# Optimization experiments

Hardware: AMD Instinct MI355X
Metric: run time of the kernel (lower is better)

## Reference

```python
import jax, jax.numpy as jnp
import numpy as np

ALPHA = 0.2  # LeakyReLU negative slope


def setup_inputs() -> dict:
    key = jax.random.key(0)
    k1, k2, k3, k4 = jax.random.split(key, 4)
    B, N, F_IN, F_OUT = 4, 4096, 256, 256
    h = jax.random.normal(k1, (B, N, F_IN), dtype=jnp.float32)
    adj = jax.random.randint(k2, (B, N, N), 0, 2, dtype=jnp.int32)
    # xavier_normal with gain=1.414: std = gain*sqrt(2/(fan_in+fan_out))
    std_W = 1.414 * np.sqrt(2.0 / (F_IN + F_OUT))
    W = jax.random.normal(k3, (F_IN, F_OUT), dtype=jnp.float32) * std_W
    std_a = 1.414 * np.sqrt(2.0 / (1 + 2 * F_OUT))
    a = jax.random.normal(k4, (1, 2 * F_OUT), dtype=jnp.float32) * std_a
    return {"h": h, "adj": adj, "W": W, "a": a}


def reference(h, adj, W, a):
    # h: [B, N, F_in], adj: [B, N, N] (0/1), W: [F_in, F_out], a: [1, 2*F_out]
    F_out = W.shape[1]
    Hh = jnp.einsum('bni,io->bno', h, W)               # [B, N, F_out]
    a_src = a[0, :F_out]                                # attends to edge source i
    a_dst = a[0, F_out:]                                # attends to edge target j
    s = jnp.einsum('bno,o->bn', Hh, a_src)              # [B, N]
    d = jnp.einsum('bno,o->bn', Hh, a_dst)              # [B, N]
    # score(i,j) = a . concat(Hh_i, Hh_j) = s_i + d_j
    logits = s[:, :, None] + d[:, None, :]              # [B, N, N]
    # edge_e = exp(-leakyrelu(score)) only on edges (adj nonzero), else 0
    e = jnp.where(adj != 0,
                  jnp.exp(-jax.nn.leaky_relu(logits, negative_slope=ALPHA)),
                  jnp.zeros((), dtype=Hh.dtype))        # [B, N, N]
    rowsum = jnp.sum(e, axis=-1, keepdims=True)         # [B, N, 1]
    # rows with zero sum keep divisor 1 (as in the torch code)
    rowsum = jnp.where(rowsum == 0.0, 1.0, rowsum)
    h_prime = jnp.einsum('bnm,bmo->bno', e, Hh) / rowsum  # [B, N, F_out]
    return jax.nn.elu(h_prime)  # concat=True branch
```

## Files before the change

### kernel.cpp

```cpp
#include <hip/hip_runtime.h>

#define LRELU_ALPHA 0.2f

typedef __bf16 bf16x8 __attribute__((ext_vector_type(8)));
typedef unsigned short u16;
typedef unsigned short u16x4v __attribute__((ext_vector_type(4)));
typedef unsigned short u16x8 __attribute__((ext_vector_type(8)));
typedef float f32x4 __attribute__((ext_vector_type(4)));
typedef int int4v __attribute__((ext_vector_type(4)));
typedef unsigned int u32;

__device__ __forceinline__ u16 f2bf(float f) {
  unsigned int u = __float_as_uint(f);
  u += 0x7fffu + ((u >> 16) & 1u);
  return (u16)(u >> 16);
}

__device__ __forceinline__ void gload16(const void* g, void* lds) {
  __builtin_amdgcn_global_load_lds(
      (const __attribute__((address_space(1))) void*)g,
      (__attribute__((address_space(3))) void*)lds, 16, 0, 0);
}

__global__ __launch_bounds__(256) void wcast(const float* __restrict__ W,
                                             u16* __restrict__ WbT) {
  int idx = blockIdx.x * 256 + threadIdx.x;
  WbT[idx] = f2bf(W[(idx & 255) * 256 + (idx >> 8)]);
}

__global__ __launch_bounds__(256) void packadj(const int* __restrict__ adj,
                                               u32* __restrict__ maskg) {
  __shared__ unsigned char nib[1024];
  const int tid = threadIdx.x;
  const size_t row0 = (size_t)blockIdx.x * 8;
  for (int rr = 0; rr < 8; ++rr) {
    const size_t row = row0 + rr;
    const int* arow = adj + row * 4096;
    for (int it = 0; it < 4; ++it) {
      int4v v = *(const int4v*)(arow + it * 1024 + tid * 4);
      unsigned char nb = (unsigned char)((v.x != 0) | ((v.y != 0) << 1) |
                                         ((v.z != 0) << 2) | ((v.w != 0) << 3));
      nib[tid] = nb;
      __syncthreads();
      if (tid < 32) {
        const u32* nw = (const u32*)nib;
        u32 w0 = nw[tid * 2], w1 = nw[tid * 2 + 1];
        u32 m = (w0 & 0xFu) | ((w0 >> 4) & 0xF0u) | ((w0 >> 8) & 0xF00u) |
                ((w0 >> 12) & 0xF000u);
        m |= ((w1 & 0xFu) | ((w1 >> 4) & 0xF0u) | ((w1 >> 8) & 0xF00u) |
              ((w1 >> 12) & 0xF000u)) << 16;
        maskg[row * 128 + it * 32 + tid] = m;
      }
      __syncthreads();
    }
  }
}

__global__ __launch_bounds__(256) void gemm1(const float* __restrict__ h,
                                             const u16* __restrict__ WbT,
                                             const float* __restrict__ a,
                                             u16* __restrict__ HhTt,
                                             float* __restrict__ sbuf,
                                             float* __restrict__ dbuf) {
  const int tid = threadIdx.x, bid = blockIdx.x;
  const int l = tid & 63, w = tid >> 6;
  const int lr = l & 15;
  const int lk = (l >> 4) << 3;
  const int rowA = bid * 64 + 16 * w + lr;
  const float* hrow = h + (size_t)rowA * 256 + lk;

  f32x4 acc[16];
#pragma unroll
  for (int n = 0; n < 16; ++n) acc[n] = (f32x4){0.f, 0.f, 0.f, 0.f};

  for (int k0 = 0; k0 < 256; k0 += 32) {
    f32x4 a0 = *(const f32x4*)(hrow + k0);
    f32x4 a1 = *(const f32x4*)(hrow + k0 + 4);
    u16x8 au;
    au[0] = f2bf(a0[0]); au[1] = f2bf(a0[1]); au[2] = f2bf(a0[2]); au[3] = f2bf(a0[3]);
    au[4] = f2bf(a1[0]); au[5] = f2bf(a1[1]); au[6] = f2bf(a1[2]); au[7] = f2bf(a1[3]);
    bf16x8 af = __builtin_bit_cast(bf16x8, au);
#pragma unroll
    for (int n = 0; n < 16; ++n) {
      int4v bv = *(const int4v*)(WbT + (size_t)(16 * n + lr) * 256 + k0 + lk);
      bf16x8 bf = __builtin_bit_cast(bf16x8, bv);
      acc[n] = __builtin_amdgcn_mfma_f32_16x16x32_bf16(af, bf, acc[n], 0, 0, 0);
    }
  }

  float sp[4] = {0.f, 0.f, 0.f, 0.f}, dp[4] = {0.f, 0.f, 0.f, 0.f};
#pragma unroll
  for (int n = 0; n < 16; ++n) {
    int col = 16 * n + lr;
    float as = a[col];
    float ad = a[256 + col];
#pragma unroll
    for (int rr = 0; rr < 4; ++rr) {
      int row = bid * 64 + 16 * w + ((l >> 4) << 2) + rr;
      int bb = row >> 12, kk = row & 4095;
      float v = acc[n][rr];
      size_t addr = (size_t)bb * 1048576 + (size_t)(kk >> 5) * 8192 +
                    (col >> 4) * 512 + ((kk >> 3) & 3) * 128 + (col & 15) * 8 +
                    (kk & 7);
      HhTt[addr] = f2bf(v);
      sp[rr] += v * as;
      dp[rr] += v * ad;
    }
  }
#pragma unroll
  for (int rr = 0; rr < 4; ++rr) {
#pragma unroll
    for (int off = 1; off < 16; off <<= 1) {
      sp[rr] += __shfl_xor(sp[rr], off);
      dp[rr] += __shfl_xor(dp[rr], off);
    }
  }
  if ((l & 15) == 0) {
#pragma unroll
    for (int rr = 0; rr < 4; ++rr) {
      int row = bid * 64 + 16 * w + ((l >> 4) << 2) + rr;
      sbuf[row] = sp[rr];
      dbuf[row] = dp[rr];
    }
  }
}

__global__ __launch_bounds__(512, 2) void gat_main(const u32* __restrict__ maskg,
                                                   const u16* __restrict__ HhTt,
                                                   const float* __restrict__ s,
                                                   const float* __restrict__ d,
                                                   float* __restrict__ out) {
  __shared__ __align__(16) u16 Bt[4][8192];
  __shared__ __align__(16) u16 At[2][2048];
  __shared__ __align__(16) u32 Mk[8192];
  __shared__ __align__(16) float Dl[4096];
  __shared__ float rs_lds[64];

  const int tid = threadIdx.x, bid = blockIdx.x;
  const int xcd = bid & 7;
  const int t256 = (xcd << 5) | (bid >> 3);
  const int b = t256 >> 6;
  const int rowbase = (t256 & 63) << 6;

  const int l = tid & 63, w = tid >> 6;
  const int lr = l & 15, lkg = l >> 4;
  const int wr = w & 1, wc = w >> 1;

  for (int i = tid; i < 1024; i += 512)
    *(f32x4*)&Dl[i * 4] = *(const f32x4*)(d + b * 4096 + i * 4);
  {
    const u32* mrow = maskg + (size_t)(b * 4096 + rowbase) * 128;
    int r = tid >> 3, w0 = (tid & 7) * 16;
#pragma unroll
    for (int j = 0; j < 16; ++j) {
      int ww = w0 + j;
      Mk[r * 128 + ((ww + r) & 127)] = mrow[r * 128 + ww];
    }
  }

  const int er = tid >> 3, c8 = tid & 7;
  const float s_e = s[b * 4096 + rowbase + er];

  const char* bsrc0 = (const char*)HhTt +
      ((size_t)b * 1048576 + (2 * w + 0) * 512 + l * 8) * 2;
  const char* bsrc1 = (const char*)HhTt +
      ((size_t)b * 1048576 + (2 * w + 1) * 512 + l * 8) * 2;
  char* BtB = (char*)&Bt[0][0];

  const int atoff0 = (32 * wr + lr) * 32 + lkg * 8;
  const int atoff1 = (32 * wr + 16 + lr) * 32 + lkg * 8;
  const int btoff = 4 * wc * 512 + lkg * 128 + lr * 8;

  f32x4 acc0[4], acc1[4];
#pragma unroll
  for (int n = 0; n < 4; ++n) {
    acc0[n] = (f32x4){0.f, 0.f, 0.f, 0.f};
    acc1[n] = (f32x4){0.f, 0.f, 0.f, 0.f};
  }
  float racc = 0.f;

#define ISSUE(BUF, STEP)                                                      \
  {                                                                           \
    const size_t so_ = (size_t)(STEP) * 16384;                                \
    gload16(bsrc0 + so_, BtB + (BUF) * 16384 + (2 * w + 0) * 1024);           \
    gload16(bsrc1 + so_, BtB + (BUF) * 16384 + (2 * w + 1) * 1024);           \
  }

#define EGEN(BUFA, STEP)                                                      \
  {                                                                           \
    const int st_ = (STEP);                                                   \
    u32 mword = Mk[er * 128 + ((st_ + er) & 127)];                            \
    u32 m8 = mword >> (c8 * 4);                                               \
    f32x4 dv = *(const f32x4*)&Dl[st_ * 32 + c8 * 4];                         \
    u16x4v ev;                                                                \
    _Pragma("unroll")                                                         \
    for (int j = 0; j < 4; ++j) {                                             \
      float lg = s_e + dv[j];                                                 \
      float t = fmaxf(lg, LRELU_ALPHA * lg);                                  \
      float e = ((m8 >> j) & 1) ? __expf(-t) : 0.f;                           \
      racc += e;                                                              \
      ev[j] = f2bf(e);                                                        \
    }                                                                         \
    *(u16x4v*)&At[BUFA][er * 32 + c8 * 4] = ev;                               \
  }

#define COMPUTE(BUFB, BUFA)                                                   \
  {                                                                           \
    bf16x8 af0 = __builtin_bit_cast(bf16x8,                                   \
        *(const int4v*)&At[BUFA][atoff0]);                                    \
    bf16x8 af1 = __builtin_bit_cast(bf16x8,                                   \
        *(const int4v*)&At[BUFA][atoff1]);                                    \
    _Pragma("unroll")                                                         \
    for (int n = 0; n < 4; ++n) {                                             \
      bf16x8 bfv = __builtin_bit_cast(bf16x8,                                 \
          *(const int4v*)&Bt[BUFB][btoff + n * 512]);                         \
      acc0[n] = __builtin_amdgcn_mfma_f32_16x16x32_bf16(af0, bfv, acc0[n],    \
                                                        0, 0, 0);             \
      acc1[n] = __builtin_amdgcn_mfma_f32_16x16x32_bf16(af1, bfv, acc1[n],    \
                                                        0, 0, 0);             \
    }                                                                         \
  }

#define WAITS(VN)                                                             \
    asm volatile("s_waitcnt lgkmcnt(0)" ::: "memory");                        \
    asm volatile("s_waitcnt vmcnt(" #VN ")" ::: "memory");                    \
    __builtin_amdgcn_s_barrier();

  ISSUE(0, 0)
  ISSUE(1, 1)
  ISSUE(2, 2)
  __syncthreads();
  EGEN(0, 0)
  asm volatile("s_waitcnt lgkmcnt(0)" ::: "memory");
  __builtin_amdgcn_s_barrier();

  for (int k = 0; k < 124; k += 4) {
    ISSUE(3, k + 3) EGEN(1, k + 1) COMPUTE(0, 0) WAITS(4)
    ISSUE(0, k + 4) EGEN(0, k + 2) COMPUTE(1, 1) WAITS(4)
    ISSUE(1, k + 5) EGEN(1, k + 3) COMPUTE(2, 0) WAITS(4)
    ISSUE(2, k + 6) EGEN(0, k + 4) COMPUTE(3, 1) WAITS(4)
  }
  ISSUE(3, 127) EGEN(1, 125) COMPUTE(0, 0) WAITS(4)
  EGEN(0, 126) COMPUTE(1, 1) WAITS(2)
  EGEN(1, 127) COMPUTE(2, 0) WAITS(0)
  COMPUTE(3, 1)
#undef ISSUE
#undef EGEN
#undef COMPUTE
#undef WAITS

  racc += __shfl_xor(racc, 1);
  racc += __shfl_xor(racc, 2);
  racc += __shfl_xor(racc, 4);
  if (c8 == 0) rs_lds[er] = (racc == 0.f) ? 1.f : racc;
  __syncthreads();

#pragma unroll
  for (int t16 = 0; t16 < 2; ++t16) {
#pragma unroll
    for (int n = 0; n < 4; ++n) {
#pragma unroll
      for (int reg = 0; reg < 4; ++reg) {
        int rloc = 32 * wr + 16 * t16 + lkg * 4 + reg;
        int col = 64 * wc + 16 * n + lr;
        float v = (t16 ? acc1[n][reg] : acc0[n][reg]) / rs_lds[rloc];
        out[((size_t)(b * 4096 + rowbase + rloc)) * 256 + col] =
            v > 0.f ? v : (__expf(v) - 1.f);
      }
    }
  }
}

extern "C" void kernel_launch(void* const* d_in, const int* in_sizes, int n_in,
                              void* d_out, int out_size, void* d_ws, size_t ws_size,
                              hipStream_t stream) {
  const float* h = (const float*)d_in[0];
  const int* adj = (const int*)d_in[1];
  const float* W = (const float*)d_in[2];
  const float* a = (const float*)d_in[3];
  float* out = (float*)d_out;

  u16* WbT   = (u16*)d_ws;
  u16* HhTt  = (u16*)((char*)d_ws + 131072);
  float* sb  = (float*)((char*)d_ws + 131072 + 8388608);
  float* db  = sb + 16384;
  u32* maskg = (u32*)((char*)d_ws + 131072 + 8388608 + 131072);

  hipLaunchKernelGGL(wcast,    dim3(256),  dim3(256), 0, stream, W, WbT);
  hipLaunchKernelGGL(packadj,  dim3(2048), dim3(256), 0, stream, adj, maskg);
  hipLaunchKernelGGL(gemm1,    dim3(256),  dim3(256), 0, stream, h, WbT, a, HhTt, sb, db);
  hipLaunchKernelGGL(gat_main, dim3(256),  dim3(512), 0, stream, maskg, HhTt, sb, db, out);
}
```

Measured before the change: 165.8 us.

## Rewrite adjacency packing with ballots and retile GAT main kernel to 32-row blocks

The adjacency bit-packing kernel now uses wave ballots to build 64-bit masks directly, one wave per row, instead of building nibbles in LDS behind repeated block barriers. The main attention kernel is retiled from 64-row, 512-thread blocks to 32-row, 256-thread blocks across twice as many blocks. It uses a triple-buffered B pipeline, streams the d vector per step into a small LDS ring instead of preloading all of it, and raises wave priority around the MFMAs. This is meant to cut packing overhead and LDS footprint to improve occupancy and SM coverage, at the cost of loading Hh twice as often overall (less reuse per block).

```diff
diff --git a/kernel.cpp b/kernel.cpp
--- a/kernel.cpp
+++ b/kernel.cpp
@@ -9,6 +9,7 @@
 typedef float f32x4 __attribute__((ext_vector_type(4)));
 typedef int int4v __attribute__((ext_vector_type(4)));
 typedef unsigned int u32;
+typedef unsigned long long u64;
 
 __device__ __forceinline__ u16 f2bf(float f) {
   unsigned int u = __float_as_uint(f);
@@ -30,28 +31,23 @@
 
 __global__ __launch_bounds__(256) void packadj(const int* __restrict__ adj,
                                                u32* __restrict__ maskg) {
-  __shared__ unsigned char nib[1024];
   const int tid = threadIdx.x;
-  const size_t row0 = (size_t)blockIdx.x * 8;
-  for (int rr = 0; rr < 8; ++rr) {
-    const size_t row = row0 + rr;
-    const int* arow = adj + row * 4096;
-    for (int it = 0; it < 4; ++it) {
-      int4v v = *(const int4v*)(arow + it * 1024 + tid * 4);
-      unsigned char nb = (unsigned char)((v.x != 0) | ((v.y != 0) << 1) |
-                                         ((v.z != 0) << 2) | ((v.w != 0) << 3));
-      nib[tid] = nb;
-      __syncthreads();
-      if (tid < 32) {
-        const u32* nw = (const u32*)nib;
-        u32 w0 = nw[tid * 2], w1 = nw[tid * 2 + 1];
-        u32 m = (w0 & 0xFu) | ((w0 >> 4) & 0xF0u) | ((w0 >> 8) & 0xF00u) |
-                ((w0 >> 12) & 0xF000u);
-        m |= ((w1 & 0xFu) | ((w1 >> 4) & 0xF0u) | ((w1 >> 8) & 0xF00u) |
-              ((w1 >> 12) & 0xF000u)) << 16;
-        maskg[row * 128 + it * 32 + tid] = m;
-      }
-      __syncthreads();
+  const int l = tid & 63, w = tid >> 6;
+  const size_t row = (size_t)blockIdx.x * 4 + w;
+  const int* arow = adj + row * 4096;
+  u64* mrow = (u64*)(maskg + row * 128);
+  for (int it = 0; it < 16; ++it) {
+    const int* base = arow + it * 256;
+    int v0 = base[l], v1 = base[l + 64], v2 = base[l + 128], v3 = base[l + 192];
+    u64 b0 = __ballot(v0 != 0);
+    u64 b1 = __ballot(v1 != 0);
+    u64 b2 = __ballot(v2 != 0);
+    u64 b3 = __ballot(v3 != 0);
+    if (l == 0) {
+      mrow[it * 4 + 0] = b0;
+      mrow[it * 4 + 1] = b1;
+      mrow[it * 4 + 2] = b2;
+      mrow[it * 4 + 3] = b3;
     }
   }
 }
@@ -125,32 +121,31 @@
   }
 }
 
-__global__ __launch_bounds__(512, 2) void gat_main(const u32* __restrict__ maskg,
+__global__ __launch_bounds__(256, 2) void gat_main(const u32* __restrict__ maskg,
                                                    const u16* __restrict__ HhTt,
                                                    const float* __restrict__ s,
                                                    const float* __restrict__ d,
                                                    float* __restrict__ out) {
-  __shared__ __align__(16) u16 Bt[4][8192];
-  __shared__ __align__(16) u16 At[2][2048];
-  __shared__ __align__(16) u32 Mk[8192];
-  __shared__ __align__(16) float Dl[4096];
-  __shared__ float rs_lds[64];
+  __shared__ __align__(16) u16 Bt[3][8192];
+  __shared__ __align__(16) u16 At[2][1024];
+  __shared__ __align__(16) u32 Mk[4096];
+  __shared__ __align__(16) float Dt[3][32];
+  __shared__ float rs_lds[32];
 
   const int tid = threadIdx.x, bid = blockIdx.x;
   const int xcd = bid & 7;
-  const int t256 = (xcd << 5) | (bid >> 3);
-  const int b = t256 >> 6;
-  const int rowbase = (t256 & 63) << 6;
+  const int t512 = (xcd << 6) | (bid >> 3);
+  const int b = t512 >> 7;
+  const int rowbase = (t512 & 127) << 5;
 
   const int l = tid & 63, w = tid >> 6;
   const int lr = l & 15, lkg = l >> 4;
-  const int wr = w & 1, wc = w >> 1;
-
-  for (int i = tid; i < 1024; i += 512)
-    *(f32x4*)&Dl[i * 4] = *(const f32x4*)(d + b * 4096 + i * 4);
+  const int er = tid >> 3, c8 = tid & 7;
+
   {
-    const u32* mrow = maskg + (size_t)(b * 4096 + rowbase) * 128;
-    int r = tid >> 3, w0 = (tid & 7) * 16;
+    const u32* mrow = maskg + ((size_t)(b * 4096 + rowbase)) * 128;
+    const int r = tid >> 3;
+    const int w0 = (tid & 7) * 16;
 #pragma unroll
     for (int j = 0; j < 16; ++j) {
       int ww = w0 + j;
@@ -158,18 +153,16 @@
     }
   }
 
-  const int er = tid >> 3, c8 = tid & 7;
   const float s_e = s[b * 4096 + rowbase + er];
 
-  const char* bsrc0 = (const char*)HhTt +
-      ((size_t)b * 1048576 + (2 * w + 0) * 512 + l * 8) * 2;
-  const char* bsrc1 = (const char*)HhTt +
-      ((size_t)b * 1048576 + (2 * w + 1) * 512 + l * 8) * 2;
+  const char* bsrcB = (const char*)HhTt + (size_t)b * 2097152 + l * 16;
+  const char* dsrcB = (const char*)d + (size_t)b * 16384 + w * 32 + l * 16;
   char* BtB = (char*)&Bt[0][0];
-
-  const int atoff0 = (32 * wr + lr) * 32 + lkg * 8;
-  const int atoff1 = (32 * wr + 16 + lr) * 32 + lkg * 8;
-  const int btoff = 4 * wc * 512 + lkg * 128 + lr * 8;
+  char* DtB = (char*)&Dt[0][0];
+
+  const int atoff0 = lr * 32 + lkg * 8;
+  const int atoff1 = (16 + lr) * 32 + lkg * 8;
+  const int btbase = (w * 4) * 512 + lkg * 128 + lr * 8;
 
   f32x4 acc0[4], acc1[4];
 #pragma unroll
@@ -179,75 +172,113 @@
   }
   float racc = 0.f;
 
-#define ISSUE(BUF, STEP)                                                      \
+#define ISSUE_B(BUF, STEP)                                                    \
   {                                                                           \
     const size_t so_ = (size_t)(STEP) * 16384;                                \
-    gload16(bsrc0 + so_, BtB + (BUF) * 16384 + (2 * w + 0) * 1024);           \
-    gload16(bsrc1 + so_, BtB + (BUF) * 16384 + (2 * w + 1) * 1024);           \
-  }
-
-#define EGEN(BUFA, STEP)                                                      \
-  {                                                                           \
-    const int st_ = (STEP);                                                   \
-    u32 mword = Mk[er * 128 + ((st_ + er) & 127)];                            \
-    u32 m8 = mword >> (c8 * 4);                                               \
-    f32x4 dv = *(const f32x4*)&Dl[st_ * 32 + c8 * 4];                         \
+    gload16(bsrcB + so_ + (w * 4 + 0) * 1024,                                 \
+            BtB + (BUF) * 16384 + (w * 4 + 0) * 1024);                        \
+    gload16(bsrcB + so_ + (w * 4 + 1) * 1024,                                 \
+            BtB + (BUF) * 16384 + (w * 4 + 1) * 1024);                        \
+    gload16(bsrcB + so_ + (w * 4 + 2) * 1024,                                 \
+            BtB + (BUF) * 16384 + (w * 4 + 2) * 1024);                        \
+    gload16(bsrcB + so_ + (w * 4 + 3) * 1024,                                 \
+            BtB + (BUF) * 16384 + (w * 4 + 3) * 1024);                        \
+  }
+
+#define ISSUE_D(STEP)                                                         \
+  {                                                                           \
+    const int dst_ = (STEP) > 127 ? 127 : (STEP);                             \
+    if (l < 2) gload16(dsrcB + (size_t)dst_ * 128,                            \
+                       DtB + (dst_ % 3) * 128 + w * 32 + l * 16);             \
+  }
+
+#define EGEN(BA, STEP)                                                        \
+  {                                                                           \
+    u32 mword = Mk[er * 128 + (((STEP) + er) & 127)];                         \
+    u32 m4 = mword >> (c8 * 4);                                               \
+    f32x4 dv = *(const f32x4*)(DtB + ((STEP) % 3) * 128 + c8 * 16);           \
     u16x4v ev;                                                                \
     _Pragma("unroll")                                                         \
     for (int j = 0; j < 4; ++j) {                                             \
       float lg = s_e + dv[j];                                                 \
       float t = fmaxf(lg, LRELU_ALPHA * lg);                                  \
-      float e = ((m8 >> j) & 1) ? __expf(-t) : 0.f;                           \
+      float e = ((m4 >> j) & 1) ? __expf(-t) : 0.f;                           \
       racc += e;                                                              \
       ev[j] = f2bf(e);                                                        \
     }                                                                         \
-    *(u16x4v*)&At[BUFA][er * 32 + c8 * 4] = ev;                               \
-  }
-
-#define COMPUTE(BUFB, BUFA)                                                   \
-  {                                                                           \
-    bf16x8 af0 = __builtin_bit_cast(bf16x8,                                   \
-        *(const int4v*)&At[BUFA][atoff0]);                                    \
-    bf16x8 af1 = __builtin_bit_cast(bf16x8,                                   \
-        *(const int4v*)&At[BUFA][atoff1]);                                    \
+    *(u16x4v*)&At[BA][er * 32 + c8 * 4] = ev;                                 \
+  }
+
+#define COMPUTE(BB, BA)                                                       \
+  {                                                                           \
+    bf16x8 af0 = __builtin_bit_cast(bf16x8, *(const int4v*)&At[BA][atoff0]);  \
+    bf16x8 af1 = __builtin_bit_cast(bf16x8, *(const int4v*)&At[BA][atoff1]);  \
+    __builtin_amdgcn_s_setprio(1);                                            \
     _Pragma("unroll")                                                         \
     for (int n = 0; n < 4; ++n) {                                             \
       bf16x8 bfv = __builtin_bit_cast(bf16x8,                                 \
-          *(const int4v*)&Bt[BUFB][btoff + n * 512]);                         \
+          *(const int4v*)&Bt[BB][btbase + n * 512]);                          \
       acc0[n] = __builtin_amdgcn_mfma_f32_16x16x32_bf16(af0, bfv, acc0[n],    \
                                                         0, 0, 0);             \
       acc1[n] = __builtin_amdgcn_mfma_f32_16x16x32_bf16(af1, bfv, acc1[n],    \
                                                         0, 0, 0);             \
     }                                                                         \
-  }
-
-#define WAITS(VN)                                                             \
+    __builtin_amdgcn_s_setprio(0);                                            \
+  }
+
+#define SUBSTEP(J, BB, BA, BI, BAN)                                           \
+  {                                                                           \
+    ISSUE_B(BI, (J) + 2)                                                      \
+    ISSUE_D((J) + 3)                                                          \
+    EGEN(BAN, (J) + 1)                                                        \
+    COMPUTE(BB, BA)                                                           \
     asm volatile("s_waitcnt lgkmcnt(0)" ::: "memory");                        \
-    asm volatile("s_waitcnt vmcnt(" #VN ")" ::: "memory");                    \
-    __builtin_amdgcn_s_barrier();
-
-  ISSUE(0, 0)
-  ISSUE(1, 1)
-  ISSUE(2, 2)
+    asm volatile("s_waitcnt vmcnt(5)" ::: "memory");                          \
+    __builtin_amdgcn_s_barrier();                                             \
+  }
+
+  ISSUE_B(0, 0)
+  ISSUE_B(1, 1)
+  ISSUE_D(1)
+  ISSUE_D(2)
+  f32x4 d0v = *(const f32x4*)(d + b * 4096 + c8 * 4);
   __syncthreads();
-  EGEN(0, 0)
+  {
+    u32 mword = Mk[er * 128 + (er & 127)];
+    u32 m4 = mword >> (c8 * 4);
+    u16x4v ev;
+#pragma unroll
+    for (int j = 0; j < 4; ++j) {
+      float lg = s_e + d0v[j];
+      float t = fmaxf(lg, LRELU_ALPHA * lg);
+      float e = ((m4 >> j) & 1) ? __expf(-t) : 0.f;
+      racc += e;
+      ev[j] = f2bf(e);
+    }
+    *(u16x4v*)&At[0][er * 32 + c8 * 4] = ev;
+  }
   asm volatile("s_waitcnt lgkmcnt(0)" ::: "memory");
   __builtin_amdgcn_s_barrier();
 
-  for (int k = 0; k < 124; k += 4) {
-    ISSUE(3, k + 3) EGEN(1, k + 1) COMPUTE(0, 0) WAITS(4)
-    ISSUE(0, k + 4) EGEN(0, k + 2) COMPUTE(1, 1) WAITS(4)
-    ISSUE(1, k + 5) EGEN(1, k + 3) COMPUTE(2, 0) WAITS(4)
-    ISSUE(2, k + 6) EGEN(0, k + 4) COMPUTE(3, 1) WAITS(4)
-  }
-  ISSUE(3, 127) EGEN(1, 125) COMPUTE(0, 0) WAITS(4)
-  EGEN(0, 126) COMPUTE(1, 1) WAITS(2)
-  EGEN(1, 127) COMPUTE(2, 0) WAITS(0)
-  COMPUTE(3, 1)
-#undef ISSUE
+  for (int k = 0; k < 126; k += 6) {
+    SUBSTEP(k + 0, 0, 0, 2, 1)
+    SUBSTEP(k + 1, 1, 1, 0, 0)
+    SUBSTEP(k + 2, 2, 0, 1, 1)
+    SUBSTEP(k + 3, 0, 1, 2, 0)
+    SUBSTEP(k + 4, 1, 0, 0, 1)
+    SUBSTEP(k + 5, 2, 1, 1, 0)
+  }
+  EGEN(1, 127)
+  COMPUTE(0, 0)
+  asm volatile("s_waitcnt lgkmcnt(0)" ::: "memory");
+  asm volatile("s_waitcnt vmcnt(0)" ::: "memory");
+  __builtin_amdgcn_s_barrier();
+  COMPUTE(1, 1)
+#undef ISSUE_B
+#undef ISSUE_D
 #undef EGEN
 #undef COMPUTE
-#undef WAITS
+#undef SUBSTEP
 
   racc += __shfl_xor(racc, 1);
   racc += __shfl_xor(racc, 2);
@@ -261,8 +292,8 @@
     for (int n = 0; n < 4; ++n) {
 #pragma unroll
       for (int reg = 0; reg < 4; ++reg) {
-        int rloc = 32 * wr + 16 * t16 + lkg * 4 + reg;
-        int col = 64 * wc + 16 * n + lr;
+        int rloc = 16 * t16 + lkg * 4 + reg;
+        int col = w * 64 + 16 * n + lr;
         float v = (t16 ? acc1[n][reg] : acc0[n][reg]) / rs_lds[rloc];
         out[((size_t)(b * 4096 + rowbase + rloc)) * 256 + col] =
             v > 0.f ? v : (__expf(v) - 1.f);
@@ -287,7 +318,7 @@
   u32* maskg = (u32*)((char*)d_ws + 131072 + 8388608 + 131072);
 
   hipLaunchKernelGGL(wcast,    dim3(256),  dim3(256), 0, stream, W, WbT);
-  hipLaunchKernelGGL(packadj,  dim3(2048), dim3(256), 0, stream, adj, maskg);
+  hipLaunchKernelGGL(packadj,  dim3(4096), dim3(256), 0, stream, adj, maskg);
   hipLaunchKernelGGL(gemm1,    dim3(256),  dim3(256), 0, stream, h, WbT, a, HhTt, sb, db);
-  hipLaunchKernelGGL(gat_main, dim3(256),  dim3(512), 0, stream, maskg, HhTt, sb, db, out);
-}
+  hipLaunchKernelGGL(gat_main, dim3(512),  dim3(256), 0, stream, maskg, HhTt, sb, db, out);
+}
```

New measurement: 170.2 us. 2.7% more time.
